# Performance work log

Measured on AMD Instinct MI355X. Metric: run time of the kernel, lower is better.

## Reference

```python
import jax, jax.numpy as jnp
import numpy as np

C = 65536      # curvenum
L = 256        # points per curve (equal-length segments)
N = C * L
FG = 4         # num_FGs
KELVIN = 273.15
FIT_AP_CI = 500.0
TARGET_R = 0.7


def setup_inputs() -> dict:
    key = jax.random.key(0)
    ks = jax.random.split(key, 16)
    f = jnp.float32
    inp = {
        "An_o": jax.random.normal(ks[0], (N,), f),
        "Ac_o": jax.random.normal(ks[1], (N,), f),
        "Aj_o": jax.random.normal(ks[2], (N,), f),
        "Ap_o": jax.random.normal(ks[3], (N,), f),
        "A_r": jax.random.normal(ks[4], (N,), f),
        "Ci": jax.random.uniform(ks[5], (N,), f) * 1000.0,
        "Vcmax25": jax.random.normal(ks[6], (C,), f),
        "Jmax25": jax.random.normal(ks[7], (C,), f),
        "Rd25": jax.random.normal(ks[8], (C,), f),
        "dHa_Vcmax": jax.random.normal(ks[9], (FG,), f),
        "dHa_Jmax": jax.random.normal(ks[10], (FG,), f),
        "dHa_TPU": jax.random.normal(ks[11], (FG,), f),
        "Topt_Vcmax": jax.random.normal(ks[12], (FG,), f) + 300.0,
        "Topt_Jmax": jax.random.normal(ks[13], (FG,), f) + 300.0,
        "Topt_TPU": jax.random.normal(ks[14], (FG,), f) + 300.0,
        "mask_lightresp": jax.random.randint(ks[15], (C,), 0, 2, jnp.int32),
    }
    return inp


def reference(An_o, Ac_o, Aj_o, Ap_o, A_r, Ci, Vcmax25, Jmax25, Rd25,
              dHa_Vcmax, dHa_Jmax, dHa_TPU, Topt_Vcmax, Topt_Jmax, Topt_TPU,
              mask_lightresp):
    relu = jax.nn.relu
    # MSE term
    loss = jnp.mean(jnp.square(An_o - A_r)) * 10.0

    # correlation penalty over non-light-response curves (curvenum > 6)
    w = (mask_lightresp == 0).astype(An_o.dtype)  # mask_nolightresp as weights
    nw = jnp.sum(w)
    y, x = Vcmax25, Jmax25
    my = jnp.sum(w * y) / nw
    mx = jnp.sum(w * x) / nw
    vy = (y - my) * w
    vx = (x - mx) * w
    cost = jnp.sum(vx * vy) / (jnp.sqrt(jnp.sum(vx * vx)) * jnp.sqrt(jnp.sum(vy * vy)))
    cost = jnp.where(jnp.isnan(cost), jnp.zeros_like(cost), cost)
    cost = jnp.minimum(cost, TARGET_R)
    loss = loss + (TARGET_R - cost)

    # sign penalties on parameters (curvenum > 1, TempResponse.type == 2, num_FGs > 1)
    loss = loss + jnp.sum(relu(-Rd25))
    loss = loss + jnp.sum(relu(-dHa_Vcmax)) * 10.0
    loss = loss + jnp.sum(relu(-dHa_Jmax))
    loss = loss + jnp.sum(relu(-dHa_TPU))
    loss = loss + jnp.sum(relu(KELVIN - Topt_Vcmax))
    loss = loss + jnp.sum(relu(KELVIN - Topt_Jmax))
    loss = loss + jnp.sum(relu(KELVIN - Topt_TPU))

    loss = loss + jnp.sum(relu(-Ap_o))

    # end-of-curve penalties
    end_idx = jnp.arange(C, dtype=jnp.int32) * L + (L - 1)
    mask_fitAp = ((Ci[end_idx] > FIT_AP_CI) & (mask_lightresp == 0)).astype(An_o.dtype)
    loss = loss + jnp.sum(relu(Ap_o[end_idx] - Aj_o[end_idx]) * mask_fitAp) * 0.15
    loss = loss + jnp.sum(relu(Aj_o[end_idx] - Ac_o[end_idx]))

    # per-curve segmented argmin + masked sums (vectorized over the C segments)
    Acj = (Ac_o - Aj_o).reshape(C, L)
    idx = jnp.argmin(jnp.abs(Acj), axis=1)  # [C] index of Ac~Aj crossover per curve
    Aj_inter = jnp.take_along_axis(Aj_o.reshape(C, L), idx[:, None], axis=1)[:, 0]
    Ap_inter = jnp.take_along_axis(Ap_o.reshape(C, L), idx[:, None], axis=1)[:, 0]
    penalty = jnp.sum(3.0 * relu(Aj_inter * 1.1 - Ap_inter))
    ls_Aj = jnp.sum(relu(-Acj), axis=1)  # sum of relu(Aj - Ac) per curve
    ls_Ac = jnp.sum(relu(Acj), axis=1)   # sum of relu(Ac - Aj) per curve
    penalty = penalty + jnp.sum(w * (relu(8.0 - ls_Aj) + relu(8.0 - ls_Ac)))

    return loss + penalty
```

## Files before the change

kernel.cpp:

```cpp
#include <hip/hip_runtime.h>
#include <math.h>

#define NC   65536
#define NL   256
#define NTOT (NC * NL)
#define WPB  4
#define CPW  8
#define NBLK (NC / (WPB * CPW))
#define NSTAT 7


typedef float vf4 __attribute__((ext_vector_type(4)));
__device__ __forceinline__ float4 ldnt4(const float* p) {
    vf4 v = __builtin_nontemporal_load((const vf4*)p);
    float4 r; r.x = v.x; r.y = v.y; r.z = v.z; r.w = v.w;
    return r;
}

__global__ __launch_bounds__(256, 4) void loss_main(
    const float* __restrict__ An, const float* __restrict__ Ac,
    const float* __restrict__ Aj, const float* __restrict__ Ap,
    const float* __restrict__ Ar, const float* __restrict__ Ci,
    const float* __restrict__ Vc, const float* __restrict__ Jm,
    const float* __restrict__ Rd, const int* __restrict__ msk,
    float* __restrict__ ws)
{
    const int lane = threadIdx.x & 63;
    const int wid  = threadIdx.x >> 6;
    const int c0   = (blockIdx.x * WPB + wid) * CPW;

    float sq = 0.f, rAp = 0.f, pen = 0.f;
    float sw=0.f, sx=0.f, sy=0.f, sxy=0.f, sxx=0.f, syy=0.f;

    float4 anA, arA, acA, ajA, apA, anB, arB, acB, ajB, apB;
    int   mA,  mB;
    float xA, yA, rdA, ciA, xB, yB, rdB, ciB;

#define LOADT(S, c) { const size_t o = (size_t)(c) * NL + (size_t)(lane << 2); \
        an##S = ldnt4(An + o);            ar##S = ldnt4(Ar + o);               \
        ac##S = *(const float4*)(Ac + o); aj##S = *(const float4*)(Aj + o);    \
        ap##S = *(const float4*)(Ap + o); }
#define LOADS(S, c) { m##S = msk[c]; x##S = Jm[c]; y##S = Vc[c];               \
        rd##S = Rd[c];                                                         \
        ci##S = __builtin_nontemporal_load(Ci + (size_t)(c) * NL + (NL - 1)); }

    auto process = [&](const float4& an, const float4& ar, const float4& ac,
                       const float4& aj, const float4& ap, int m, float xv,
                       float yv, float rd, float ci) {
        float d;
        d = an.x - ar.x; sq = fmaf(d, d, sq);
        d = an.y - ar.y; sq = fmaf(d, d, sq);
        d = an.z - ar.z; sq = fmaf(d, d, sq);
        d = an.w - ar.w; sq = fmaf(d, d, sq);

        float lsAj = 0.f, lsAc = 0.f;
        unsigned key = 0xFFFFFFFFu;
#define COMP(ACV, AJV, APV, J)                                                 \
        { rAp += fmaxf(-(APV), 0.f);                                           \
          float acj = (ACV) - (AJV);                                           \
          lsAj += fmaxf(-acj, 0.f); lsAc += fmaxf(acj, 0.f);                   \
          unsigned kb = (__float_as_uint(fabsf(acj)) & 0xFFFFFF00u)            \
                        | (unsigned)((lane << 2) + (J));                       \
          key = key < kb ? key : kb; }
        COMP(ac.x, aj.x, ap.x, 0)
        COMP(ac.y, aj.y, ap.y, 1)
        COMP(ac.z, aj.z, ap.z, 2)
        COMP(ac.w, aj.w, ap.w, 3)
#undef COMP

#pragma unroll
        for (int s = 1; s < 64; s <<= 1) {
            unsigned ok = __shfl_xor(key, s);
            key = key < ok ? key : ok;
            lsAj += __shfl_xor(lsAj, s);
            lsAc += __shfl_xor(lsAc, s);
        }

        const int idx = (int)(key & 255u);
        const int lo  = idx >> 2;
        const int cc  = idx & 3;
        float selA = cc==0 ? aj.x : cc==1 ? aj.y : cc==2 ? aj.z : aj.w;
        float selP = cc==0 ? ap.x : cc==1 ? ap.y : cc==2 ? ap.z : ap.w;
        const float aj_at = __shfl(selA, lo);
        const float ap_at = __shfl(selP, lo);

        const float wm = (m == 0) ? 1.f : 0.f;
        const float fw = (ci > 500.f) ? 0.15f * wm : 0.f;
        if (lane == 0) {
            pen += 3.f * fmaxf(1.1f * aj_at - ap_at, 0.f);
            pen += wm * (fmaxf(8.f - lsAj, 0.f) + fmaxf(8.f - lsAc, 0.f));
            pen += fmaxf(-rd, 0.f);
            sw += wm;      sx += wm * xv;       sy += wm * yv;
            sxy = fmaf(wm * xv, yv, sxy);
            sxx = fmaf(wm * xv, xv, sxx);
            syy = fmaf(wm * yv, yv, syy);
        }
        if (lane == 63) {
            pen += fmaxf(aj.w - ac.w, 0.f);
            pen += fw * fmaxf(ap.w - aj.w, 0.f);
        }
    };

    LOADT(A, c0) LOADS(A, c0)
#pragma unroll 1
    for (int k = 0; k < CPW; k += 2) {
        LOADT(B, c0 + k + 1) LOADS(B, c0 + k + 1)
        process(anA, arA, acA, ajA, apA, mA, xA, yA, rdA, ciA);
        if (k + 2 < CPW) { LOADT(A, c0 + k + 2) LOADS(A, c0 + k + 2) }
        process(anB, arB, acB, ajB, apB, mB, xB, yB, rdB, ciB);
    }
#undef LOADT
#undef LOADS

    float A = fmaf(sq, 10.f / (float)NTOT, rAp + pen);
#pragma unroll
    for (int s = 1; s < 64; s <<= 1) A += __shfl_xor(A, s);

    __shared__ float sred[WPB][NSTAT];
    if (lane == 0) {
        sred[wid][0] = A;   sred[wid][1] = sw;  sred[wid][2] = sx;
        sred[wid][3] = sy;  sred[wid][4] = sxy; sred[wid][5] = sxx;
        sred[wid][6] = syy;
    }
    __syncthreads();
    if (threadIdx.x == 0) {
#pragma unroll
        for (int j = 0; j < NSTAT; ++j) {
            float v = sred[0][j] + sred[1][j] + sred[2][j] + sred[3][j];
            ws[j * NBLK + blockIdx.x] = v;
        }
    }
}

__global__ __launch_bounds__(256) void loss_final(
    const float* __restrict__ ws,
    const float* __restrict__ dHaV, const float* __restrict__ dHaJ,
    const float* __restrict__ dHaT,
    const float* __restrict__ ToV,  const float* __restrict__ ToJ,
    const float* __restrict__ ToT,
    float* __restrict__ out)
{
    __shared__ float red[NSTAT][256];
    const int t = threadIdx.x;
    float p[NSTAT];
#pragma unroll
    for (int j = 0; j < NSTAT; ++j) p[j] = 0.f;
    for (int k = 0; k < NBLK / 256; ++k) {
        int b = t + k * 256;
#pragma unroll
        for (int j = 0; j < NSTAT; ++j) p[j] += ws[j * NBLK + b];
    }
#pragma unroll
    for (int j = 0; j < NSTAT; ++j) red[j][t] = p[j];
    __syncthreads();
    for (int s = 128; s > 0; s >>= 1) {
        if (t < s) {
#pragma unroll
            for (int j = 0; j < NSTAT; ++j) red[j][t] += red[j][t + s];
        }
        __syncthreads();
    }
    if (t == 0) {
        float A   = red[0][0];
        float sw  = red[1][0], sx  = red[2][0], sy  = red[3][0];
        float sxy = red[4][0], sxx = red[5][0], syy = red[6][0];

        float loss = A;

        float cnum = sxy - sx * sy / sw;
        float cden = sqrtf(sxx - sx * sx / sw) * sqrtf(syy - sy * sy / sw);
        float cost = cnum / cden;
        if (!(cost == cost)) cost = 0.f;
        cost = fminf(cost, 0.7f);
        loss += 0.7f - cost;

        float fg = 0.f;
#pragma unroll
        for (int i = 0; i < 4; ++i) {
            fg += 10.f * fmaxf(-dHaV[i], 0.f);
            fg += fmaxf(-dHaJ[i], 0.f);
            fg += fmaxf(-dHaT[i], 0.f);
            fg += fmaxf(273.15f - ToV[i], 0.f);
            fg += fmaxf(273.15f - ToJ[i], 0.f);
            fg += fmaxf(273.15f - ToT[i], 0.f);
        }
        loss += fg;

        out[0] = loss;
    }
}

extern "C" void kernel_launch(void* const* d_in, const int* in_sizes, int n_in,
                              void* d_out, int out_size, void* d_ws, size_t ws_size,
                              hipStream_t stream) {
    const float* An  = (const float*)d_in[0];
    const float* Ac  = (const float*)d_in[1];
    const float* Aj  = (const float*)d_in[2];
    const float* Ap  = (const float*)d_in[3];
    const float* Ar  = (const float*)d_in[4];
    const float* Ci  = (const float*)d_in[5];
    const float* Vc  = (const float*)d_in[6];
    const float* Jm  = (const float*)d_in[7];
    const float* Rd  = (const float*)d_in[8];
    const float* dHaV = (const float*)d_in[9];
    const float* dHaJ = (const float*)d_in[10];
    const float* dHaT = (const float*)d_in[11];
    const float* ToV  = (const float*)d_in[12];
    const float* ToJ  = (const float*)d_in[13];
    const float* ToT  = (const float*)d_in[14];
    const int*   msk  = (const int*)d_in[15];

    float* ws  = (float*)d_ws;
    float* out = (float*)d_out;

    loss_main<<<NBLK, 256, 0, stream>>>(An, Ac, Aj, Ap, Ar, Ci, Vc, Jm, Rd, msk, ws);
    loss_final<<<1, 256, 0, stream>>>(ws, dHaV, dHaJ, dHaT, ToV, ToJ, ToT, out);
}
```

Baseline: 58.97 us.

## Stage Ac/Aj/Ap through LDS with async global-to-LDS loads, deeper prefetch

Replaces register double-buffering with a four-deep pipeline. An/Ar still load into registers, while Ac/Aj/Ap go straight to LDS through global_load_lds and are throttled by explicit vmcnt waits. Per-curve scalars (mask, Jm, Vc, Rd, Ci end) are loaded once up front, one lane per curve, and reduced with shuffles. The aim is more bytes in flight per wave to hide HBM latency on this bandwidth-bound stream. The cost is LDS use, occupancy hint lowered from 4 to 3, and fragile hand-counted waitcnt values.

```diff
diff --git a/kernel.cpp b/kernel.cpp
--- a/kernel.cpp
+++ b/kernel.cpp
@@ -17,7 +17,13 @@
     return r;
 }
 
-__global__ __launch_bounds__(256, 4) void loss_main(
+__device__ __forceinline__ void gl_lds16(const float* g, float* l) {
+    __builtin_amdgcn_global_load_lds(
+        (const __attribute__((address_space(1))) float*)g,
+        (__attribute__((address_space(3))) float*)l, 16, 0, 0);
+}
+
+__global__ __launch_bounds__(256, 3) void loss_main(
     const float* __restrict__ An, const float* __restrict__ Ac,
     const float* __restrict__ Aj, const float* __restrict__ Ap,
     const float* __restrict__ Ar, const float* __restrict__ Ci,
@@ -25,6 +31,9 @@
     const float* __restrict__ Rd, const int* __restrict__ msk,
     float* __restrict__ ws)
 {
+    __shared__ float ldsb[WPB][4][3][NL];
+    __shared__ float sred[WPB][NSTAT];
+
     const int lane = threadIdx.x & 63;
     const int wid  = threadIdx.x >> 6;
     const int c0   = (blockIdx.x * WPB + wid) * CPW;
@@ -32,29 +41,30 @@
     float sq = 0.f, rAp = 0.f, pen = 0.f;
     float sw=0.f, sx=0.f, sy=0.f, sxy=0.f, sxx=0.f, syy=0.f;
 
-    float4 anA, arA, acA, ajA, apA, anB, arB, acB, ajB, apB;
-    int   mA,  mB;
-    float xA, yA, rdA, ciA, xB, yB, rdB, ciB;
-
-#define LOADT(S, c) { const size_t o = (size_t)(c) * NL + (size_t)(lane << 2); \
-        an##S = ldnt4(An + o);            ar##S = ldnt4(Ar + o);               \
-        ac##S = *(const float4*)(Ac + o); aj##S = *(const float4*)(Aj + o);    \
-        ap##S = *(const float4*)(Ap + o); }
-#define LOADS(S, c) { m##S = msk[c]; x##S = Jm[c]; y##S = Vc[c];               \
-        rd##S = Rd[c];                                                         \
-        ci##S = __builtin_nontemporal_load(Ci + (size_t)(c) * NL + (NL - 1)); }
-
-    auto process = [&](const float4& an, const float4& ar, const float4& ac,
-                       const float4& aj, const float4& ap, int m, float xv,
-                       float yv, float rd, float ci) {
-        float d;
-        d = an.x - ar.x; sq = fmaf(d, d, sq);
-        d = an.y - ar.y; sq = fmaf(d, d, sq);
-        d = an.z - ar.z; sq = fmaf(d, d, sq);
-        d = an.w - ar.w; sq = fmaf(d, d, sq);
-
-        float lsAj = 0.f, lsAc = 0.f;
-        unsigned key = 0xFFFFFFFFu;
+    float wmask = 0.f, fitw = 0.f;
+    if (lane < CPW) {
+        const int cc2 = c0 + lane;
+        const int m = msk[cc2];
+        const float x = Jm[cc2], y = Vc[cc2], rd = Rd[cc2];
+        const float ci = __builtin_nontemporal_load(Ci + (size_t)cc2 * NL + (NL - 1));
+        const float wm = (m == 0) ? 1.f : 0.f;
+        wmask = wm;
+        fitw  = (ci > 500.f) ? 0.15f * wm : 0.f;
+        pen   = fmaxf(-rd, 0.f);
+        sw = wm; sx = wm * x; sy = wm * y;
+        sxy = wm * x * y; sxx = wm * x * x; syy = wm * y * y;
+    }
+    asm volatile("s_waitcnt vmcnt(0)" ::: "memory");
+
+    float4 an0, an1, an2, an3, ar0, ar1, ar2, ar3;
+
+#define STAGE(S, c) {                                                          \
+        const size_t o_ = (size_t)(c) * NL + (size_t)(lane << 2);              \
+        an##S = ldnt4(An + o_);  ar##S = ldnt4(Ar + o_);                       \
+        gl_lds16(Ac + o_, &ldsb[wid][S][0][0]);                                \
+        gl_lds16(Aj + o_, &ldsb[wid][S][1][0]);                                \
+        gl_lds16(Ap + o_, &ldsb[wid][S][2][0]); }
+
 #define COMP(ACV, AJV, APV, J)                                                 \
         { rAp += fmaxf(-(APV), 0.f);                                           \
           float acj = (ACV) - (AJV);                                           \
@@ -62,61 +72,85 @@
           unsigned kb = (__float_as_uint(fabsf(acj)) & 0xFFFFFF00u)            \
                         | (unsigned)((lane << 2) + (J));                       \
           key = key < kb ? key : kb; }
-        COMP(ac.x, aj.x, ap.x, 0)
-        COMP(ac.y, aj.y, ap.y, 1)
-        COMP(ac.z, aj.z, ap.z, 2)
-        COMP(ac.w, aj.w, ap.w, 3)
+
+#define PROCESS(an, ar, ac, aj, ap, kk) {                                      \
+        float d;                                                               \
+        d = an.x - ar.x; sq = fmaf(d, d, sq);                                  \
+        d = an.y - ar.y; sq = fmaf(d, d, sq);                                  \
+        d = an.z - ar.z; sq = fmaf(d, d, sq);                                  \
+        d = an.w - ar.w; sq = fmaf(d, d, sq);                                  \
+        float lsAj = 0.f, lsAc = 0.f;                                          \
+        unsigned key = 0xFFFFFFFFu;                                            \
+        COMP(ac.x, aj.x, ap.x, 0)                                              \
+        COMP(ac.y, aj.y, ap.y, 1)                                              \
+        COMP(ac.z, aj.z, ap.z, 2)                                              \
+        COMP(ac.w, aj.w, ap.w, 3)                                              \
+        _Pragma("unroll")                                                      \
+        for (int s = 1; s < 64; s <<= 1) {                                     \
+            unsigned ok = __shfl_xor(key, s);                                  \
+            key = key < ok ? key : ok;                                         \
+            lsAj += __shfl_xor(lsAj, s);                                       \
+            lsAc += __shfl_xor(lsAc, s);                                       \
+        }                                                                      \
+        const int idx = (int)(key & 255u);                                     \
+        const int lo  = idx >> 2;                                              \
+        const int cc  = idx & 3;                                               \
+        float selA = cc==0 ? aj.x : cc==1 ? aj.y : cc==2 ? aj.z : aj.w;        \
+        float selP = cc==0 ? ap.x : cc==1 ? ap.y : cc==2 ? ap.z : ap.w;        \
+        const float aj_at = __shfl(selA, lo);                                  \
+        const float ap_at = __shfl(selP, lo);                                  \
+        const float wv = __shfl(wmask, kk);                                    \
+        const float fw = __shfl(fitw,  kk);                                    \
+        if (lane == 0) {                                                       \
+            pen += 3.f * fmaxf(1.1f * aj_at - ap_at, 0.f);                     \
+            pen += wv * (fmaxf(8.f - lsAj, 0.f) + fmaxf(8.f - lsAc, 0.f));     \
+        }                                                                      \
+        if (lane == 63) {                                                      \
+            pen += fmaxf(aj.w - ac.w, 0.f);                                    \
+            pen += fw * fmaxf(ap.w - aj.w, 0.f);                               \
+        } }
+
+#define ITER(S, W, STAGE_STMT, kk) {                                           \
+        asm volatile("s_waitcnt vmcnt(" #W ")" ::: "memory");                  \
+        const int li_ = lane << 2;                                             \
+        float4 ac = *(const float4*)&ldsb[wid][S][0][li_];                     \
+        float4 aj = *(const float4*)&ldsb[wid][S][1][li_];                     \
+        float4 ap = *(const float4*)&ldsb[wid][S][2][li_];                     \
+        asm volatile("s_waitcnt lgkmcnt(0)" ::: "memory");                     \
+        STAGE_STMT;                                                            \
+        PROCESS(an##S, ar##S, ac, aj, ap, kk) }
+
+    STAGE(0, c0 + 0)
+    STAGE(1, c0 + 1)
+    STAGE(2, c0 + 2)
+    STAGE(3, c0 + 3)
+
+    ITER(0, 15, STAGE(0, c0 + 4), 0)
+    ITER(1, 15, STAGE(1, c0 + 5), 1)
+    ITER(2, 15, STAGE(2, c0 + 6), 2)
+    ITER(3, 15, STAGE(3, c0 + 7), 3)
+    ITER(0, 15, , 4)
+    ITER(1, 10, , 5)
+    ITER(2, 5,  , 6)
+    ITER(3, 0,  , 7)
+
+#undef ITER
+#undef PROCESS
 #undef COMP
-
-#pragma unroll
-        for (int s = 1; s < 64; s <<= 1) {
-            unsigned ok = __shfl_xor(key, s);
-            key = key < ok ? key : ok;
-            lsAj += __shfl_xor(lsAj, s);
-            lsAc += __shfl_xor(lsAc, s);
-        }
-
-        const int idx = (int)(key & 255u);
-        const int lo  = idx >> 2;
-        const int cc  = idx & 3;
-        float selA = cc==0 ? aj.x : cc==1 ? aj.y : cc==2 ? aj.z : aj.w;
-        float selP = cc==0 ? ap.x : cc==1 ? ap.y : cc==2 ? ap.z : ap.w;
-        const float aj_at = __shfl(selA, lo);
-        const float ap_at = __shfl(selP, lo);
-
-        const float wm = (m == 0) ? 1.f : 0.f;
-        const float fw = (ci > 500.f) ? 0.15f * wm : 0.f;
-        if (lane == 0) {
-            pen += 3.f * fmaxf(1.1f * aj_at - ap_at, 0.f);
-            pen += wm * (fmaxf(8.f - lsAj, 0.f) + fmaxf(8.f - lsAc, 0.f));
-            pen += fmaxf(-rd, 0.f);
-            sw += wm;      sx += wm * xv;       sy += wm * yv;
-            sxy = fmaf(wm * xv, yv, sxy);
-            sxx = fmaf(wm * xv, xv, sxx);
-            syy = fmaf(wm * yv, yv, syy);
-        }
-        if (lane == 63) {
-            pen += fmaxf(aj.w - ac.w, 0.f);
-            pen += fw * fmaxf(ap.w - aj.w, 0.f);
-        }
-    };
-
-    LOADT(A, c0) LOADS(A, c0)
-#pragma unroll 1
-    for (int k = 0; k < CPW; k += 2) {
-        LOADT(B, c0 + k + 1) LOADS(B, c0 + k + 1)
-        process(anA, arA, acA, ajA, apA, mA, xA, yA, rdA, ciA);
-        if (k + 2 < CPW) { LOADT(A, c0 + k + 2) LOADS(A, c0 + k + 2) }
-        process(anB, arB, acB, ajB, apB, mB, xB, yB, rdB, ciB);
-    }
-#undef LOADT
-#undef LOADS
+#undef STAGE
 
     float A = fmaf(sq, 10.f / (float)NTOT, rAp + pen);
 #pragma unroll
-    for (int s = 1; s < 64; s <<= 1) A += __shfl_xor(A, s);
-
-    __shared__ float sred[WPB][NSTAT];
+    for (int s = 1; s < 64; s <<= 1) {
+        A   += __shfl_xor(A,   s);
+        sw  += __shfl_xor(sw,  s);
+        sx  += __shfl_xor(sx,  s);
+        sy  += __shfl_xor(sy,  s);
+        sxy += __shfl_xor(sxy, s);
+        sxx += __shfl_xor(sxx, s);
+        syy += __shfl_xor(syy, s);
+    }
+
     if (lane == 0) {
         sred[wid][0] = A;   sred[wid][1] = sw;  sred[wid][2] = sx;
         sred[wid][3] = sy;  sred[wid][4] = sxy; sred[wid][5] = sxx;
```

New measurement: 51.20 us. 1.15x faster.
